# Optimization experiments

Hardware: AMD Instinct MI355X
Metric: run time of the kernel (lower is better)

Reference implementation:

```python
import jax, jax.numpy as jnp
import numpy as np

MAX_SEQ_LEN = 65536
DISCOUNT_FACTOR = 0.99
ADVANTAGE_LAMBDA = 0.95


def _init_lambda_sequence(target_mean, seq_len):
    # mirrors LearnableTD._create_init_lambda_sequence
    initial = 2.0 * target_mean - 1.0
    final = 1.0
    if initial < 0:
        initial = 0.0
        final = 2.0 * target_mean
    lam = np.zeros(seq_len, dtype=np.float32)
    lam[:-1] = np.linspace(initial, final, seq_len - 1, dtype=np.float32)
    lam[-1] = 1.0
    # clip so atanh stays finite (torch atanh(1.0) -> inf)
    return np.clip(lam, 0.0, 1.0 - 1e-6)


def setup_inputs() -> dict:
    lam = _init_lambda_sequence(ADVANTAGE_LAMBDA, MAX_SEQ_LEN)
    raw_gamma = jnp.arctanh(jnp.full((1,), DISCOUNT_FACTOR, dtype=jnp.float32))
    raw_lambd = jnp.arctanh(jnp.asarray(lam, dtype=jnp.float32))
    return {"raw_gamma": raw_gamma, "raw_lambd": raw_lambd}


def reference(raw_gamma, raw_lambd):
    # LearnableTD.update_sum_reward_weights
    gamma = jnp.maximum(jnp.tanh(raw_gamma), 0.0)[0]      # scalar
    lambd = jnp.maximum(jnp.tanh(raw_lambd), 0.0)          # [S]

    # backward affine recurrence: v_t = gamma*(1 - l_t + l_t * v_{t+1}), v_S = 1
    def step(v_next, l_t):
        v_t = gamma * (1.0 - l_t + l_t * v_next)
        w_t = jnp.maximum(1.0 - v_t, 1e-8)
        return v_t, w_t

    _, raw_w = jax.lax.scan(step, jnp.float32(1.0), lambd, reverse=True)
    raw_w = raw_w[None, :, None]                            # [1, S, 1]
    scale = 1.0 / jnp.maximum(jnp.mean(raw_w), 1e-8)
    return scale * raw_w
```

## Files before the change

### kernel.cpp

```cpp
#include <hip/hip_runtime.h>

#define N_ELEMS 65536
#define NBLK    64
#define BTH     1024
#define NWAVE   (BTH / 64)
#define CHK     0x5F3759DFu


__device__ __forceinline__ float fast_tanh_pos(float x) {
    const float t = __expf(2.0f * x);
    return (t - 1.0f) * __builtin_amdgcn_rcpf(t + 1.0f);
}

__device__ __forceinline__ void wave_suffix_scan(float& A, float& B, int lane) {
#pragma unroll
    for (int d = 1; d < 64; d <<= 1) {
        const float A2 = __shfl_down(A, d, 64);
        const float B2 = __shfl_down(B, d, 64);
        if (lane + d < 64) { B = fmaf(A, B2, B); A = A * A2; }
    }
}

__device__ __forceinline__ unsigned long long pack_chk(float f) {
    const unsigned u = __float_as_uint(f);
    return (unsigned long long)u | ((unsigned long long)(u ^ CHK) << 32);
}

__device__ __forceinline__ void pub_store(unsigned long long* p,
                                          unsigned long long v) {
    __hip_atomic_store(p, v, __ATOMIC_RELAXED, __HIP_MEMORY_SCOPE_AGENT);
}
__device__ __forceinline__ unsigned long long pub_load(
        const unsigned long long* p) {
    return __hip_atomic_load(p, __ATOMIC_RELAXED, __HIP_MEMORY_SCOPE_AGENT);
}

__global__ __launch_bounds__(BTH) void fused_td_kernel(
        const float* __restrict__ raw_gamma,
        const float* __restrict__ raw_lambd,
        float* __restrict__ out,
        unsigned long long* __restrict__ pub) {
    const int tid  = threadIdx.x;
    const int lane = tid & 63;
    const int w    = tid >> 6;
    const int bid  = blockIdx.x;

    __shared__ float sA[NWAVE], sB[NWAVE], sSA[NWAVE], sSB[NWAVE];
    __shared__ float sVblk, sScale;

    const float gamma = fmaxf(fast_tanh_pos(raw_gamma[0]), 0.0f);

    const int g = bid * BTH + tid;
    const float lam = fmaxf(fast_tanh_pos(raw_lambd[g]), 0.0f);
    const float a   = gamma * lam;

    float A = a, B = gamma - a;
    wave_suffix_scan(A, B, lane);
    if (lane == 0) { sA[w] = A; sB[w] = B; }
    __syncthreads();

    float tA[NWAVE], tB[NWAVE];
#pragma unroll
    for (int j = 0; j < NWAVE; ++j) { tA[j] = sA[j]; tB[j] = sB[j]; }
    float TA = 1.0f, TB = 0.0f;
#pragma unroll
    for (int j = 0; j < NWAVE; ++j) {
        if (j > w) { TB = fmaf(TA, tB[j], TB); TA *= tA[j]; }
    }
    const float fA = A * TA;
    const float fB = fmaf(A, TB, B);

    float rA = fA, rB = fB;
#pragma unroll
    for (int off = 32; off > 0; off >>= 1) {
        rA += __shfl_down(rA, off, 64);
        rB += __shfl_down(rB, off, 64);
    }
    if (lane == 0) { sSA[w] = rA; sSB[w] = rB; }
    __syncthreads();

    if (tid == 0) {
        float bSA = 0.0f, bSB = 0.0f;
#pragma unroll
        for (int j = 0; j < NWAVE; ++j) { bSA += sSA[j]; bSB += sSB[j]; }
        pub_store(&pub[0 * NBLK + bid], pack_chk(fA));
        pub_store(&pub[1 * NBLK + bid], pack_chk(fB));
        pub_store(&pub[2 * NBLK + bid], pack_chk(bSA));
        pub_store(&pub[3 * NBLK + bid], pack_chk(bSB));
    }

    if (w == 0) {
        float bA, bB, cSA, cSB;
        for (;;) {
            const unsigned long long q0 = pub_load(&pub[0 * NBLK + lane]);
            const unsigned long long q1 = pub_load(&pub[1 * NBLK + lane]);
            const unsigned long long q2 = pub_load(&pub[2 * NBLK + lane]);
            const unsigned long long q3 = pub_load(&pub[3 * NBLK + lane]);
            const bool ok =
                ((unsigned)(q0 >> 32) == ((unsigned)q0 ^ CHK)) &&
                ((unsigned)(q1 >> 32) == ((unsigned)q1 ^ CHK)) &&
                ((unsigned)(q2 >> 32) == ((unsigned)q2 ^ CHK)) &&
                ((unsigned)(q3 >> 32) == ((unsigned)q3 ^ CHK));
            if (ok) {
                bA  = __uint_as_float((unsigned)q0);
                bB  = __uint_as_float((unsigned)q1);
                cSA = __uint_as_float((unsigned)q2);
                cSB = __uint_as_float((unsigned)q3);
                break;
            }
            __builtin_amdgcn_s_sleep(2);
        }

        wave_suffix_scan(bA, bB, lane);
        const float S   = bA + bB;
        float vin = __shfl_down(S, 1, 64);
        if (lane == 63) vin = 1.0f;

        float term = fmaf(cSA, vin, cSB);
#pragma unroll
        for (int off = 32; off > 0; off >>= 1)
            term += __shfl_xor(term, off, 64);
        const float mean_w = ((float)N_ELEMS - term) * (1.0f / (float)N_ELEMS);
        const float scale  = 1.0f / fmaxf(mean_w, 1e-8f);
        const float v_blk  = __shfl(vin, bid, 64);

        if (lane == 0) { sVblk = v_blk; sScale = scale; }
    }
    __syncthreads();

    const float v  = fmaf(fA, sVblk, fB);
    const float wq = fmaxf(1.0f - v, 1e-8f);
    out[g] = sScale * wq;
}

extern "C" void kernel_launch(void* const* d_in, const int* in_sizes, int n_in,
                              void* d_out, int out_size, void* d_ws, size_t ws_size,
                              hipStream_t stream) {
    const float* raw_gamma = (const float*)d_in[0];
    const float* raw_lambd = (const float*)d_in[1];
    float* out = (float*)d_out;
    unsigned long long* pub = (unsigned long long*)d_ws;

    fused_td_kernel<<<NBLK, BTH, 0, stream>>>(raw_gamma, raw_lambd, out, pub);
}
```

Baseline: 10.53 us.

## Process four elements per thread with serial local scan and float4 I/O

Shrinks blocks from 1024 to 256 threads, and each thread now loads four lambdas with a float4. It composes them serially into a local affine transform and running sums before the wave scan, then recomputes the four outputs serially and writes them with a float4. This cuts the number of waves taking part in the intra-block scan and barriers, and shortens the cross-wave combine. The spin-wait sleep is also reduced. The cost is more serial work per thread and a longer dependent chain.

```diff
diff --git a/kernel.cpp b/kernel.cpp
--- a/kernel.cpp
+++ b/kernel.cpp
@@ -2,7 +2,8 @@
 
 #define N_ELEMS 65536
 #define NBLK    64
-#define BTH     1024
+#define BTH     256
+#define EPT     4
 #define NWAVE   (BTH / 64)
 #define CHK     0x5F3759DFu
 
@@ -25,7 +26,6 @@
     const unsigned u = __float_as_uint(f);
     return (unsigned long long)u | ((unsigned long long)(u ^ CHK) << 32);
 }
-
 __device__ __forceinline__ void pub_store(unsigned long long* p,
                                           unsigned long long v) {
     __hip_atomic_store(p, v, __ATOMIC_RELAXED, __HIP_MEMORY_SCOPE_AGENT);
@@ -50,39 +50,49 @@
 
     const float gamma = fmaxf(fast_tanh_pos(raw_gamma[0]), 0.0f);
 
-    const int g = bid * BTH + tid;
-    const float lam = fmaxf(fast_tanh_pos(raw_lambd[g]), 0.0f);
-    const float a   = gamma * lam;
+    const int c = bid * BTH + tid;
+    const float4 r = *reinterpret_cast<const float4*>(raw_lambd + 4 * c);
+    const float a0 = gamma * fmaxf(fast_tanh_pos(r.x), 0.0f);
+    const float a1 = gamma * fmaxf(fast_tanh_pos(r.y), 0.0f);
+    const float a2 = gamma * fmaxf(fast_tanh_pos(r.z), 0.0f);
+    const float a3 = gamma * fmaxf(fast_tanh_pos(r.w), 0.0f);
 
-    float A = a, B = gamma - a;
-    wave_suffix_scan(A, B, lane);
-    if (lane == 0) { sA[w] = A; sB[w] = B; }
+    float A  = a3, B = gamma - a3;
+    float SA = A,  SB = B;
+    B = fmaf(a2, B, gamma - a2); A = a2 * A; SA += A; SB += B;
+    B = fmaf(a1, B, gamma - a1); A = a1 * A; SA += A; SB += B;
+    B = fmaf(a0, B, gamma - a0); A = a0 * A; SA += A; SB += B;
+
+    float iA = A, iB = B;
+    wave_suffix_scan(iA, iB, lane);
+    if (lane == 0) { sA[w] = iA; sB[w] = iB; }
     __syncthreads();
 
-    float tA[NWAVE], tB[NWAVE];
-#pragma unroll
-    for (int j = 0; j < NWAVE; ++j) { tA[j] = sA[j]; tB[j] = sB[j]; }
     float TA = 1.0f, TB = 0.0f;
 #pragma unroll
     for (int j = 0; j < NWAVE; ++j) {
-        if (j > w) { TB = fmaf(TA, tB[j], TB); TA *= tA[j]; }
+        if (j > w) { TB = fmaf(TA, sB[j], TB); TA *= sA[j]; }
     }
-    const float fA = A * TA;
-    const float fB = fmaf(A, TB, B);
+    const float fA = iA * TA;
+    const float fB = fmaf(iA, TB, iB);
 
-    float rA = fA, rB = fB;
+    float eA = __shfl_down(fA, 1, 64);
+    float eB = __shfl_down(fB, 1, 64);
+    if (lane == 63) { eA = TA; eB = TB; }
+
+    float rSA = SA * eA;
+    float rSB = fmaf(SA, eB, SB);
 #pragma unroll
     for (int off = 32; off > 0; off >>= 1) {
-        rA += __shfl_down(rA, off, 64);
-        rB += __shfl_down(rB, off, 64);
+        rSA += __shfl_down(rSA, off, 64);
+        rSB += __shfl_down(rSB, off, 64);
     }
-    if (lane == 0) { sSA[w] = rA; sSB[w] = rB; }
+    if (lane == 0) { sSA[w] = rSA; sSB[w] = rSB; }
     __syncthreads();
 
     if (tid == 0) {
-        float bSA = 0.0f, bSB = 0.0f;
-#pragma unroll
-        for (int j = 0; j < NWAVE; ++j) { bSA += sSA[j]; bSB += sSB[j]; }
+        const float bSA = (sSA[0] + sSA[1]) + (sSA[2] + sSA[3]);
+        const float bSB = (sSB[0] + sSB[1]) + (sSB[2] + sSB[3]);
         pub_store(&pub[0 * NBLK + bid], pack_chk(fA));
         pub_store(&pub[1 * NBLK + bid], pack_chk(fB));
         pub_store(&pub[2 * NBLK + bid], pack_chk(bSA));
@@ -108,11 +118,11 @@
                 cSB = __uint_as_float((unsigned)q3);
                 break;
             }
-            __builtin_amdgcn_s_sleep(2);
+            __builtin_amdgcn_s_sleep(1);
         }
 
         wave_suffix_scan(bA, bB, lane);
-        const float S   = bA + bB;
+        const float S = bA + bB;
         float vin = __shfl_down(S, 1, 64);
         if (lane == 63) vin = 1.0f;
 
@@ -128,9 +138,18 @@
     }
     __syncthreads();
 
-    const float v  = fmaf(fA, sVblk, fB);
-    const float wq = fmaxf(1.0f - v, 1e-8f);
-    out[g] = sScale * wq;
+    const float scale = sScale;
+    const float u  = fmaf(eA, sVblk, eB);
+    const float v3 = fmaf(a3, u,  gamma - a3);
+    const float v2 = fmaf(a2, v3, gamma - a2);
+    const float v1 = fmaf(a1, v2, gamma - a1);
+    const float v0 = fmaf(a0, v1, gamma - a0);
+    float4 o;
+    o.x = scale * fmaxf(1.0f - v0, 1e-8f);
+    o.y = scale * fmaxf(1.0f - v1, 1e-8f);
+    o.z = scale * fmaxf(1.0f - v2, 1e-8f);
+    o.w = scale * fmaxf(1.0f - v3, 1e-8f);
+    *reinterpret_cast<float4*>(out + 4 * c) = o;
 }
 
 extern "C" void kernel_launch(void* const* d_in, const int* in_sizes, int n_in,
```

Result: faster. 9.881 us (-6.1%).

## Use single-wave blocks with 16 elements per thread and serial per-thread scan

Applied to the files above, without the earlier changes.

Restructures each block from 1024 threads (16 waves) to one 64-thread wave in which every thread handles 16 contiguous elements. Each thread does a serial affine scan over its elements, then one wave-level suffix scan runs, which removes the shared-memory staging and both __syncthreads barriers. Loads and stores become float4-vectorised. In exchange each thread carries a longer serial dependency chain and a recompute pass for the outputs, and far fewer waves are in flight to hide memory latency. The spin sleep is also shortened.

```diff
diff --git a/kernel.cpp b/kernel.cpp
--- a/kernel.cpp
+++ b/kernel.cpp
@@ -2,8 +2,8 @@
 
 #define N_ELEMS 65536
 #define NBLK    64
-#define BTH     1024
-#define NWAVE   (BTH / 64)
+#define BTH     64
+#define EPT     16
 #define CHK     0x5F3759DFu
 
 
@@ -25,7 +25,6 @@
     const unsigned u = __float_as_uint(f);
     return (unsigned long long)u | ((unsigned long long)(u ^ CHK) << 32);
 }
-
 __device__ __forceinline__ void pub_store(unsigned long long* p,
                                           unsigned long long v) {
     __hip_atomic_store(p, v, __ATOMIC_RELAXED, __HIP_MEMORY_SCOPE_AGENT);
@@ -40,97 +39,101 @@
         const float* __restrict__ raw_lambd,
         float* __restrict__ out,
         unsigned long long* __restrict__ pub) {
-    const int tid  = threadIdx.x;
-    const int lane = tid & 63;
-    const int w    = tid >> 6;
+    const int lane = threadIdx.x;
     const int bid  = blockIdx.x;
-
-    __shared__ float sA[NWAVE], sB[NWAVE], sSA[NWAVE], sSB[NWAVE];
-    __shared__ float sVblk, sScale;
 
     const float gamma = fmaxf(fast_tanh_pos(raw_gamma[0]), 0.0f);
 
-    const int g = bid * BTH + tid;
-    const float lam = fmaxf(fast_tanh_pos(raw_lambd[g]), 0.0f);
-    const float a   = gamma * lam;
+    const int base = (bid * BTH + lane) * EPT;
+    float a[EPT];
+#pragma unroll
+    for (int k = 0; k < EPT; k += 4) {
+        const float4 r = *reinterpret_cast<const float4*>(raw_lambd + base + k);
+        a[k + 0] = gamma * fmaxf(fast_tanh_pos(r.x), 0.0f);
+        a[k + 1] = gamma * fmaxf(fast_tanh_pos(r.y), 0.0f);
+        a[k + 2] = gamma * fmaxf(fast_tanh_pos(r.z), 0.0f);
+        a[k + 3] = gamma * fmaxf(fast_tanh_pos(r.w), 0.0f);
+    }
 
-    float A = a, B = gamma - a;
-    wave_suffix_scan(A, B, lane);
-    if (lane == 0) { sA[w] = A; sB[w] = B; }
-    __syncthreads();
+    float A  = a[EPT - 1], B = gamma - a[EPT - 1];
+    float SA = A, SB = B;
+#pragma unroll
+    for (int k = EPT - 2; k >= 0; --k) {
+        B = fmaf(a[k], B, gamma - a[k]);
+        A = a[k] * A;
+        SA += A; SB += B;
+    }
 
-    float tA[NWAVE], tB[NWAVE];
-#pragma unroll
-    for (int j = 0; j < NWAVE; ++j) { tA[j] = sA[j]; tB[j] = sB[j]; }
-    float TA = 1.0f, TB = 0.0f;
-#pragma unroll
-    for (int j = 0; j < NWAVE; ++j) {
-        if (j > w) { TB = fmaf(TA, tB[j], TB); TA *= tA[j]; }
-    }
-    const float fA = A * TA;
-    const float fB = fmaf(A, TB, B);
+    float iA = A, iB = B;
+    wave_suffix_scan(iA, iB, lane);
 
-    float rA = fA, rB = fB;
+    float eA = __shfl_down(iA, 1, 64);
+    float eB = __shfl_down(iB, 1, 64);
+    if (lane == 63) { eA = 1.0f; eB = 0.0f; }
+
+    float rSA = SA * eA;
+    float rSB = fmaf(SA, eB, SB);
 #pragma unroll
     for (int off = 32; off > 0; off >>= 1) {
-        rA += __shfl_down(rA, off, 64);
-        rB += __shfl_down(rB, off, 64);
-    }
-    if (lane == 0) { sSA[w] = rA; sSB[w] = rB; }
-    __syncthreads();
-
-    if (tid == 0) {
-        float bSA = 0.0f, bSB = 0.0f;
-#pragma unroll
-        for (int j = 0; j < NWAVE; ++j) { bSA += sSA[j]; bSB += sSB[j]; }
-        pub_store(&pub[0 * NBLK + bid], pack_chk(fA));
-        pub_store(&pub[1 * NBLK + bid], pack_chk(fB));
-        pub_store(&pub[2 * NBLK + bid], pack_chk(bSA));
-        pub_store(&pub[3 * NBLK + bid], pack_chk(bSB));
+        rSA += __shfl_down(rSA, off, 64);
+        rSB += __shfl_down(rSB, off, 64);
     }
 
-    if (w == 0) {
-        float bA, bB, cSA, cSB;
-        for (;;) {
-            const unsigned long long q0 = pub_load(&pub[0 * NBLK + lane]);
-            const unsigned long long q1 = pub_load(&pub[1 * NBLK + lane]);
-            const unsigned long long q2 = pub_load(&pub[2 * NBLK + lane]);
-            const unsigned long long q3 = pub_load(&pub[3 * NBLK + lane]);
-            const bool ok =
-                ((unsigned)(q0 >> 32) == ((unsigned)q0 ^ CHK)) &&
-                ((unsigned)(q1 >> 32) == ((unsigned)q1 ^ CHK)) &&
-                ((unsigned)(q2 >> 32) == ((unsigned)q2 ^ CHK)) &&
-                ((unsigned)(q3 >> 32) == ((unsigned)q3 ^ CHK));
-            if (ok) {
-                bA  = __uint_as_float((unsigned)q0);
-                bB  = __uint_as_float((unsigned)q1);
-                cSA = __uint_as_float((unsigned)q2);
-                cSB = __uint_as_float((unsigned)q3);
-                break;
-            }
-            __builtin_amdgcn_s_sleep(2);
+    if (lane == 0) {
+        pub_store(&pub[0 * NBLK + bid], pack_chk(iA));
+        pub_store(&pub[1 * NBLK + bid], pack_chk(iB));
+        pub_store(&pub[2 * NBLK + bid], pack_chk(rSA));
+        pub_store(&pub[3 * NBLK + bid], pack_chk(rSB));
+    }
+
+    float bA, bB, cSA, cSB;
+    for (;;) {
+        const unsigned long long q0 = pub_load(&pub[0 * NBLK + lane]);
+        const unsigned long long q1 = pub_load(&pub[1 * NBLK + lane]);
+        const unsigned long long q2 = pub_load(&pub[2 * NBLK + lane]);
+        const unsigned long long q3 = pub_load(&pub[3 * NBLK + lane]);
+        const bool ok =
+            ((unsigned)(q0 >> 32) == ((unsigned)q0 ^ CHK)) &&
+            ((unsigned)(q1 >> 32) == ((unsigned)q1 ^ CHK)) &&
+            ((unsigned)(q2 >> 32) == ((unsigned)q2 ^ CHK)) &&
+            ((unsigned)(q3 >> 32) == ((unsigned)q3 ^ CHK));
+        if (ok) {
+            bA  = __uint_as_float((unsigned)q0);
+            bB  = __uint_as_float((unsigned)q1);
+            cSA = __uint_as_float((unsigned)q2);
+            cSB = __uint_as_float((unsigned)q3);
+            break;
         }
+        __builtin_amdgcn_s_sleep(1);
+    }
 
-        wave_suffix_scan(bA, bB, lane);
-        const float S   = bA + bB;
-        float vin = __shfl_down(S, 1, 64);
-        if (lane == 63) vin = 1.0f;
+    wave_suffix_scan(bA, bB, lane);
+    const float S = bA + bB;
+    float vin = __shfl_down(S, 1, 64);
+    if (lane == 63) vin = 1.0f;
 
-        float term = fmaf(cSA, vin, cSB);
+    float term = fmaf(cSA, vin, cSB);
 #pragma unroll
-        for (int off = 32; off > 0; off >>= 1)
-            term += __shfl_xor(term, off, 64);
-        const float mean_w = ((float)N_ELEMS - term) * (1.0f / (float)N_ELEMS);
-        const float scale  = 1.0f / fmaxf(mean_w, 1e-8f);
-        const float v_blk  = __shfl(vin, bid, 64);
+    for (int off = 32; off > 0; off >>= 1)
+        term += __shfl_xor(term, off, 64);
+    const float mean_w = ((float)N_ELEMS - term) * (1.0f / (float)N_ELEMS);
+    const float scale  = 1.0f / fmaxf(mean_w, 1e-8f);
+    const float v_blk  = __shfl(vin, bid, 64);
 
-        if (lane == 0) { sVblk = v_blk; sScale = scale; }
+    const float u = fmaf(eA, v_blk, eB);
+    float o[EPT];
+    float v = u;
+#pragma unroll
+    for (int k = EPT - 1; k >= 0; --k) {
+        v = fmaf(a[k], v, gamma - a[k]);
+        o[k] = scale * fmaxf(1.0f - v, 1e-8f);
     }
-    __syncthreads();
-
-    const float v  = fmaf(fA, sVblk, fB);
-    const float wq = fmaxf(1.0f - v, 1e-8f);
-    out[g] = sScale * wq;
+#pragma unroll
+    for (int k = 0; k < EPT; k += 4) {
+        float4 w4;
+        w4.x = o[k + 0]; w4.y = o[k + 1]; w4.z = o[k + 2]; w4.w = o[k + 3];
+        *reinterpret_cast<float4*>(out + base + k) = w4;
+    }
 }
 
 extern "C" void kernel_launch(void* const* d_in, const int* in_sizes, int n_in,
```

Measured after the change: 9.947 us. 1.06x faster.
